# Kernel optimization log

Hardware: AMD Instinct MI355X
Metric: run time of the kernel (lower is better)

## Reference

```python
import jax, jax.numpy as jnp
import numpy as np

ALPHA = 0.9  # smoothing coefficient from init_kwargs


def setup_inputs() -> dict:
    key = jax.random.key(0)
    x = jax.random.normal(key, (8, 4096, 1024), dtype=jnp.float32)
    return {"x": x}


def reference(x):
    # EMA along time axis (dim=1): y_t = alpha*y_{t-1} + (1-alpha)*x_t, y_{-1}=0
    alpha = jnp.asarray(ALPHA, dtype=x.dtype)
    om_alpha = jnp.asarray(1.0 - ALPHA, dtype=x.dtype)
    xt = jnp.swapaxes(x, 0, 1)  # [T, B, F]

    def step(carry, xt_t):
        y = alpha * carry + om_alpha * xt_t
        return y, y

    y0 = jnp.zeros(xt.shape[1:], dtype=x.dtype)  # [B, F]
    _, ys = jax.lax.scan(step, y0, xt)  # ys: [T, B, F]
    return jnp.swapaxes(ys, 0, 1)  # [B, T, F]
```

## Files before the change

### kernel.cpp

```cpp
#include <hip/hip_runtime.h>


using f4 = __attribute__((ext_vector_type(4))) float;

constexpr int Bn = 8;
constexpr int Tn = 4096;
constexpr int F4 = 256;
constexpr int L  = 64;
constexpr int W  = 64;
constexpr int BATCH = 8;
constexpr float A   = 0.9f;
constexpr float OMA = 0.1f;

__global__ __launch_bounds__(256) void ema_kernel(const f4* __restrict__ x,
                                                  f4* __restrict__ y) {
    const int tid          = threadIdx.x;
    const int lane_f       = tid & 63;
    const int chunk_in_blk = tid >> 6;
    const int blk          = blockIdx.x;
    const int chunkgrp     = blk & 15;
    const int fg           = (blk >> 4) & 3;
    const int b            = blk >> 6;

    const int chunk = chunkgrp * 4 + chunk_in_blk;
    const int f4i   = (fg << 6) + lane_f;
    const int t0    = chunk * L;

    const f4* __restrict__ xp = x + (size_t)b * Tn * F4 + f4i;
    f4*       __restrict__ yp = y + (size_t)b * Tn * F4 + f4i;

    float ax = 0.f, ay = 0.f, az = 0.f, aw = 0.f;

    if (chunk > 0) {
        int idx = (t0 - W) * F4;
        for (int ii = 0; ii < W; ii += BATCH) {
            f4 v[BATCH];
            #pragma unroll
            for (int j = 0; j < BATCH; ++j) v[j] = xp[idx + j * F4];
            #pragma unroll
            for (int j = 0; j < BATCH; ++j) {
                ax = fmaf(A, ax, OMA * v[j].x);
                ay = fmaf(A, ay, OMA * v[j].y);
                az = fmaf(A, az, OMA * v[j].z);
                aw = fmaf(A, aw, OMA * v[j].w);
            }
            idx += BATCH * F4;
        }
    }

    int idx = t0 * F4;
    for (int ii = 0; ii < L; ii += BATCH) {
        f4 v[BATCH];
        #pragma unroll
        for (int j = 0; j < BATCH; ++j) v[j] = xp[idx + j * F4];
        #pragma unroll
        for (int j = 0; j < BATCH; ++j) {
            ax = fmaf(A, ax, OMA * v[j].x);
            ay = fmaf(A, ay, OMA * v[j].y);
            az = fmaf(A, az, OMA * v[j].z);
            aw = fmaf(A, aw, OMA * v[j].w);
            f4 o;
            o.x = ax; o.y = ay; o.z = az; o.w = aw;
            __builtin_nontemporal_store(o, yp + idx + j * F4);
        }
        idx += BATCH * F4;
    }
}

extern "C" void kernel_launch(void* const* d_in, const int* in_sizes, int n_in,
                              void* d_out, int out_size, void* d_ws, size_t ws_size,
                              hipStream_t stream) {
    const f4* x = (const f4*)d_in[0];
    f4*       y = (f4*)d_out;
    dim3 grid(Bn * 4 * 16);
    dim3 block(256);
    ema_kernel<<<grid, block, 0, stream>>>(x, y);
}
```

Before: 246.8 us.

## Shorten EMA chunks, widen per-thread features, and software-pipeline loads

Time chunks shrink from 64 to 16 steps while keeping the 64-step warm-up window. Each thread now carries 16 feature accumulators, four f4 columns, instead of one f4. The time loop keeps four rotating load buffers so the next rows are in flight while the current row is computed. The aim is a shorter serial recurrence chain per wave and more memory parallelism. The cost is much more redundant warm-up reading (80 rows read per 16 written), which relies on cache hits from overlapping neighbouring chunks.

```diff
diff --git a/kernel.cpp b/kernel.cpp
--- a/kernel.cpp
+++ b/kernel.cpp
@@ -6,64 +6,68 @@
 constexpr int Bn = 8;
 constexpr int Tn = 4096;
 constexpr int F4 = 256;
-constexpr int L  = 64;
+constexpr int L  = 16;
 constexpr int W  = 64;
-constexpr int BATCH = 8;
 constexpr float A   = 0.9f;
 constexpr float OMA = 0.1f;
 
 __global__ __launch_bounds__(256) void ema_kernel(const f4* __restrict__ x,
                                                   f4* __restrict__ y) {
-    const int tid          = threadIdx.x;
-    const int lane_f       = tid & 63;
-    const int chunk_in_blk = tid >> 6;
-    const int blk          = blockIdx.x;
-    const int chunkgrp     = blk & 15;
-    const int fg           = (blk >> 4) & 3;
-    const int b            = blk >> 6;
-
-    const int chunk = chunkgrp * 4 + chunk_in_blk;
-    const int f4i   = (fg << 6) + lane_f;
+    const int lane  = threadIdx.x & 63;
+    const int wave  = threadIdx.x >> 6;
+    const int blk   = blockIdx.x;
+    const int b     = blk >> 6;
+    const int chunk = ((blk & 63) << 2) | wave;
     const int t0    = chunk * L;
 
-    const f4* __restrict__ xp = x + (size_t)b * Tn * F4 + f4i;
-    f4*       __restrict__ yp = y + (size_t)b * Tn * F4 + f4i;
+    const size_t base = (size_t)b * Tn * F4 + lane;
+    const f4* __restrict__ xp = x + base;
+    f4*       __restrict__ yp = y + base;
 
-    float ax = 0.f, ay = 0.f, az = 0.f, aw = 0.f;
+    float acc[16];
+    #pragma unroll
+    for (int i = 0; i < 16; ++i) acc[i] = 0.f;
 
-    if (chunk > 0) {
-        int idx = (t0 - W) * F4;
-        for (int ii = 0; ii < W; ii += BATCH) {
-            f4 v[BATCH];
+    int ts = t0 - W;
+    if (ts < 0) ts = 0;
+    const int te = t0 + L;
+
+    auto LD = [&](f4* v, int t) {
+        const f4* __restrict__ p = xp + (size_t)t * F4;
+        #pragma unroll
+        for (int j = 0; j < 4; ++j) v[j] = p[j * 64];
+    };
+    auto STEP = [&](const f4* v, int t) {
+        #pragma unroll
+        for (int j = 0; j < 4; ++j) {
+            acc[4*j+0] = fmaf(A, acc[4*j+0], OMA * v[j].x);
+            acc[4*j+1] = fmaf(A, acc[4*j+1], OMA * v[j].y);
+            acc[4*j+2] = fmaf(A, acc[4*j+2], OMA * v[j].z);
+            acc[4*j+3] = fmaf(A, acc[4*j+3], OMA * v[j].w);
+        }
+        if (t >= t0) {
+            f4* __restrict__ p = yp + (size_t)t * F4;
             #pragma unroll
-            for (int j = 0; j < BATCH; ++j) v[j] = xp[idx + j * F4];
-            #pragma unroll
-            for (int j = 0; j < BATCH; ++j) {
-                ax = fmaf(A, ax, OMA * v[j].x);
-                ay = fmaf(A, ay, OMA * v[j].y);
-                az = fmaf(A, az, OMA * v[j].z);
-                aw = fmaf(A, aw, OMA * v[j].w);
+            for (int j = 0; j < 4; ++j) {
+                f4 o;
+                o.x = acc[4*j+0]; o.y = acc[4*j+1];
+                o.z = acc[4*j+2]; o.w = acc[4*j+3];
+                __builtin_nontemporal_store(o, p + j * 64);
             }
-            idx += BATCH * F4;
         }
-    }
+    };
 
-    int idx = t0 * F4;
-    for (int ii = 0; ii < L; ii += BATCH) {
-        f4 v[BATCH];
-        #pragma unroll
-        for (int j = 0; j < BATCH; ++j) v[j] = xp[idx + j * F4];
-        #pragma unroll
-        for (int j = 0; j < BATCH; ++j) {
-            ax = fmaf(A, ax, OMA * v[j].x);
-            ay = fmaf(A, ay, OMA * v[j].y);
-            az = fmaf(A, az, OMA * v[j].z);
-            aw = fmaf(A, aw, OMA * v[j].w);
-            f4 o;
-            o.x = ax; o.y = ay; o.z = az; o.w = aw;
-            __builtin_nontemporal_store(o, yp + idx + j * F4);
-        }
-        idx += BATCH * F4;
+    f4 v0[4], v1[4], v2[4], v3[4];
+    LD(v0, ts); LD(v1, ts + 1); LD(v2, ts + 2); LD(v3, ts + 3);
+    for (int t = ts; t < te; t += 4) {
+        STEP(v0, t);
+        if (t + 4 < te) LD(v0, t + 4);
+        STEP(v1, t + 1);
+        if (t + 5 < te) LD(v1, t + 5);
+        STEP(v2, t + 2);
+        if (t + 6 < te) LD(v2, t + 6);
+        STEP(v3, t + 3);
+        if (t + 7 < te) LD(v3, t + 7);
     }
 }
 
@@ -72,7 +76,7 @@
                               hipStream_t stream) {
     const f4* x = (const f4*)d_in[0];
     f4*       y = (f4*)d_out;
-    dim3 grid(Bn * 4 * 16);
+    dim3 grid(Bn * 64);
     dim3 block(256);
     ema_kernel<<<grid, block, 0, stream>>>(x, y);
 }
```

Result: slower. 296.2 us (+20.0%).
